# Optimization experiments

Measured on AMD Instinct MI355X. Metric: run time of the kernel, lower is better.

Reference implementation:

```python
import jax, jax.numpy as jnp
import numpy as np

LEAKY_SLOPE = 0.01
BN_EPS = 1e-5


def _local_conv(x, w, b, stride):
    # x: [B,C,H,W]; w: [1,O,C,OH,OW,K] (K = kh*kw, kh==kw); b: [1,O,OH,OW]
    sh, sw = stride
    _, O, C, oh, ow, K = w.shape
    k = int(round(K ** 0.5))
    # gather unfold patches: torch .unfold(2,kh,dh).unfold(3,kw,dw) -> last dim ordered (i major, j minor)
    patches = jnp.stack(
        [x[:, :, i:i + sh * oh:sh, j:j + sw * ow:sw] for i in range(k) for j in range(k)],
        axis=-1)  # [B,C,oh,ow,K]
    out = jnp.einsum('bchwk,ochwk->bohw', patches, w[0])
    return out + b  # b broadcasts [1,O,OH,OW]


def _bn_train(x, gamma, beta):
    # BatchNorm2d in training mode: biased batch statistics over (N,H,W)
    m = jnp.mean(x, axis=(0, 2, 3), keepdims=True)
    v = jnp.var(x, axis=(0, 2, 3), keepdims=True)
    return gamma[None, :, None, None] * (x - m) * jax.lax.rsqrt(v + BN_EPS) + beta[None, :, None, None]


def _lrelu(x):
    return jnp.where(x >= 0, x, LEAKY_SLOPE * x)


def _pad1(x):
    return jnp.pad(x, ((0, 0), (0, 0), (1, 1), (1, 1)))


def setup_inputs() -> dict:
    key = jax.random.key(0)
    ks = jax.random.split(key, 16)
    B = 8192
    inp = {
        'image': jax.random.normal(ks[0], (B, 10, 9, 1), jnp.float32),
        'conv1_w': jax.random.normal(ks[1], (64, 1, 2, 2), jnp.float32) * 0.5,
        'conv1_b': jax.random.normal(ks[2], (64,), jnp.float32) * 0.1,
        'lc1_w': jax.random.normal(ks[3], (1, 16, 64, 10, 5, 9), jnp.float32) * 0.05,
        'lc1_b': jax.random.normal(ks[4], (1, 16, 10, 5), jnp.float32) * 0.1,
        'lc2_w': jax.random.normal(ks[5], (1, 8, 16, 11, 6, 4), jnp.float32) * 0.1,
        'lc2_b': jax.random.normal(ks[6], (1, 8, 11, 6), jnp.float32) * 0.1,
        'lc3_w': jax.random.normal(ks[7], (1, 8, 8, 12, 4, 4), jnp.float32) * 0.1,
        'lc3_b': jax.random.normal(ks[8], (1, 8, 12, 4), jnp.float32) * 0.1,
        'gamma1': jax.random.normal(ks[9], (16,), jnp.float32) * 0.1 + 1.0,
        'beta1': jax.random.normal(ks[10], (16,), jnp.float32) * 0.1,
        'gamma2': jax.random.normal(ks[11], (8,), jnp.float32) * 0.1 + 1.0,
        'beta2': jax.random.normal(ks[12], (8,), jnp.float32) * 0.1,
        'gamma3': jax.random.normal(ks[13], (8,), jnp.float32) * 0.1 + 1.0,
        'beta3': jax.random.normal(ks[14], (8,), jnp.float32) * 0.1,
    }
    return inp


def reference(image, conv1_w, conv1_b, lc1_w, lc1_b, lc2_w, lc2_b, lc3_w, lc3_b,
              gamma1, beta1, gamma2, beta2, gamma3, beta3):
    x = jnp.transpose(image, (0, 3, 1, 2))  # [B,1,10,9]
    # Conv2d kernel 2, padding='same' (torch pads extra on right/bottom for even kernels)
    x = jax.lax.conv_general_dilated(
        x, conv1_w, window_strides=(1, 1), padding=[(0, 1), (0, 1)],
        dimension_numbers=('NCHW', 'OIHW', 'NCHW'))
    x = x + conv1_b[None, :, None, None]
    x = _lrelu(x)
    x = _pad1(x)                               # [B,64,12,11]
    x = _local_conv(x, lc1_w, lc1_b, (1, 2))   # [B,16,10,5]
    x = _lrelu(x)
    x = _bn_train(x, gamma1, beta1)
    x = _pad1(x)                               # [B,16,12,7]
    x = _local_conv(x, lc2_w, lc2_b, (1, 1))   # [B,8,11,6]
    x = _lrelu(x)
    x = _bn_train(x, gamma2, beta2)
    x = _pad1(x)                               # [B,8,13,8]
    x = _local_conv(x, lc3_w, lc3_b, (1, 2))   # [B,8,12,4]
    x = _lrelu(x)
    x = _bn_train(x, gamma3, beta3)
    return x.reshape(x.shape[0], -1)           # [B,384]
```

## Files before the change

### kernel.cpp

```cpp
#include <hip/hip_runtime.h>


typedef float  f32x4 __attribute__((ext_vector_type(4)));
typedef float  f32x2 __attribute__((ext_vector_type(2)));
typedef short  bf16x8 __attribute__((ext_vector_type(8)));

union FR  { int4 i4; bf16x8 bf; unsigned u[4]; };

#define LRELU(v) fmaxf((v), 0.01f * (v))

static __device__ inline unsigned bfr(float f) {
    unsigned u = __float_as_uint(f);
    return (u + 0x7fffu + ((u >> 16) & 1u)) >> 16;
}
static __device__ inline unsigned short bfr16(float f) { return (unsigned short)bfr(f); }
static __device__ inline float ubf(unsigned lo16) { return __uint_as_float(lo16 << 16); }

#if __has_builtin(__builtin_elementwise_fma)
static __device__ inline f32x2 pk_fma(f32x2 a, f32x2 b, f32x2 c) { return __builtin_elementwise_fma(a, b, c); }
#else
static __device__ inline f32x2 pk_fma(f32x2 a, f32x2 b, f32x2 c) { return a * b + c; }
#endif
static __device__ inline f32x2 pk_lrelu(f32x2 v) {
#if __has_builtin(__builtin_elementwise_max)
    return __builtin_elementwise_max(v, v * 0.01f);
#else
    f32x2 r; r.x = LRELU(v.x); r.y = LRELU(v.y); return r;
#endif
}
static __device__ inline float aload(float* p) {
    return __hip_atomic_load(p, __ATOMIC_RELAXED, __HIP_MEMORY_SCOPE_AGENT);
}

union PrepSM { float imgP[16][110]; float wt[9216]; };

__global__ __launch_bounds__(256) void kprep(
    const float* __restrict__ imgp,
    const float* __restrict__ cw,
    const float* __restrict__ cb,
    const float* __restrict__ lw1,
    unsigned* __restrict__ x1u,
    int4* __restrict__ afg1, float* __restrict__ stats,
    int nA, int doAux, int spp)
{
    __shared__ PrepSM sm;
    const int bx = blockIdx.x, tid = threadIdx.x;

    if (bx < nA) {
        const int sb = bx * 16;
        for (int e = tid; e < 1760; e += 256) ((float*)sm.imgP)[e] = 0.0f;
        __syncthreads();
        for (int e = tid; e < 1440; e += 256) {
            int s = e / 90, hw = e - s * 90;
            int r = hw / 9, c = hw - r * 9;
            sm.imgP[s][r * 10 + c] = imgp[(size_t)sb * 90 + e];
        }
        __syncthreads();

        const int quad = tid & 3, s = (tid >> 2) & 15;
        const int h = (tid >> 6) & 1, hwo = tid >> 7;
        const int ch0 = h * 32 + quad * 8;
        f32x2 W00[4], W01[4], W10[4], W11[4], BB[4];
        #pragma unroll
        for (int p = 0; p < 4; ++p) {
            int ca = ch0 + 2 * p, cbn = ca + 1;
            W00[p] = (f32x2){cw[ca * 4 + 0], cw[cbn * 4 + 0]};
            W01[p] = (f32x2){cw[ca * 4 + 1], cw[cbn * 4 + 1]};
            W10[p] = (f32x2){cw[ca * 4 + 2], cw[cbn * 4 + 2]};
            W11[p] = (f32x2){cw[ca * 4 + 3], cw[cbn * 4 + 3]};
            BB[p]  = (f32x2){cb[ca], cb[cbn]};
        }
        const float* ip = sm.imgP[s];
        uint4* x1q = (uint4*)x1u;
        #pragma unroll 3
        for (int it = 0; it < 45; ++it) {
            int hw = it * 2 + hwo;
            int r = hw / 9, c = hw - r * 9;
            float i00 = ip[r * 10 + c],      i01 = ip[r * 10 + c + 1];
            float i10 = ip[r * 10 + c + 10], i11 = ip[r * 10 + c + 11];
            unsigned u[4];
            #pragma unroll
            for (int p = 0; p < 4; ++p) {
                f32x2 v = BB[p];
                v = pk_fma((f32x2)i00, W00[p], v);
                v = pk_fma((f32x2)i01, W01[p], v);
                v = pk_fma((f32x2)i10, W10[p], v);
                v = pk_fma((f32x2)i11, W11[p], v);
                v = pk_lrelu(v);
                u[p] = bfr(v.x) | (bfr(v.y) << 16);
            }
            x1q[((size_t)(hw * 2 + h) * spp + (sb + s)) * 4 + quad] =
                make_uint4(u[0], u[1], u[2], u[3]);
        }
        return;
    }
    if (!doAux) return;

    const int b2 = bx - nA;
    if (b2 < 50) {
        const int pos = b2;
        for (int e = tid; e < 9216; e += 256) {
            int pair = e / 9, t = e - 9 * pair;
            sm.wt[e] = lw1[pair * 450 + pos * 9 + t];
        }
        __syncthreads();
        for (int e = tid; e < 1152; e += 256) {
            int l = e & 63, ht = e >> 6;
            int h = (ht >= 9) ? 1 : 0, t = ht - 9 * h;
            int q = l >> 4, o = l & 15;
            unsigned uu[4];
            #pragma unroll
            for (int p = 0; p < 4; ++p) {
                int c0 = 32 * h + 8 * q + 2 * p;
                float a0 = sm.wt[(o * 64 + c0) * 9 + t];
                float a1 = sm.wt[(o * 64 + c0 + 1) * 9 + t];
                uu[p] = bfr(a0) | (bfr(a1) << 16);
            }
            int4 st = { (int)uu[0], (int)uu[1], (int)uu[2], (int)uu[3] };
            afg1[pos * 1152 + e] = st;
        }
    } else if (tid < 64) stats[tid] = 0.0f;
}

__global__ __launch_bounds__(256) void k1_lc1(
    const int4* __restrict__ x1v,
    const int4* __restrict__ afg,
    const float* __restrict__ lb,
    unsigned short* __restrict__ y1b,
    float* __restrict__ stats,
    int sampOff, int spp, int nc)
{
    __shared__ int4  AfL[1216];
    __shared__ float bl[16];
    __shared__ float red[32];

    int pos, chunk;
    {
        int id = blockIdx.x;
        if (nc >= 8) { int k8 = id & 7; int r = id >> 3; pos = r % 50; chunk = (r / 50) * 8 + k8; }
        else         { pos = id % 50; chunk = id / 50; }
    }
    const int oh = pos / 5, ow = pos % 5;
    const int tid = threadIdx.x;
    const int wv = tid >> 6, lane = tid & 63;
    const int lane15 = lane & 15, q = lane >> 4;

    for (int e = tid; e < 1152; e += 256) AfL[e] = afg[pos * 1152 + e];
    if (tid < 64) AfL[1152 + tid] = (int4){0, 0, 0, 0};
    if (tid < 16) bl[tid] = lb[tid * 50 + pos];
    if (tid < 32) red[tid] = 0.0f;
    __syncthreads();

    const int sLoc = chunk * 256 + wv * 64;
    const int sAbs = sampOff + sLoc;
    const int spp4 = spp * 4;

    int sb0[9], af0[9], af1[9];
    #pragma unroll
    for (int t = 0; t < 9; ++t) {
        int ti = t / 3, tj = t % 3;
        int r = oh + ti - 1, c2 = 2 * ow + tj - 1;
        bool ok = (r >= 0 && r < 10 && c2 >= 0 && c2 < 9);
        int hw = ok ? (r * 9 + c2) : 0;
        sb0[t] = hw * 2 * spp4;
        af0[t] = ok ? t * 64 : 1152;
        af1[t] = ok ? (9 + t) * 64 : 1152;
    }

    f32x4 acc[4];
    #pragma unroll
    for (int g = 0; g < 4; ++g) {
        const int bg = (sLoc + g * 16 + lane15) * 4 + q;
        FR fb[9][2];
        #pragma unroll
        for (int t = 0; t < 9; ++t) {
            fb[t][0].i4 = x1v[sb0[t] + bg];
            fb[t][1].i4 = x1v[sb0[t] + spp4 + bg];
        }
        f32x4 a = (f32x4){0.f, 0.f, 0.f, 0.f};
        #pragma unroll
        for (int t = 0; t < 9; ++t) {
            FR fa0; fa0.i4 = AfL[af0[t] + lane];
            a = __builtin_amdgcn_mfma_f32_16x16x32_bf16(fa0.bf, fb[t][0].bf, a, 0, 0, 0);
            FR fa1; fa1.i4 = AfL[af1[t] + lane];
            a = __builtin_amdgcn_mfma_f32_16x16x32_bf16(fa1.bf, fb[t][1].bf, a, 0, 0, 0);
        }
        acc[g] = a;
    }

    float so[4] = {0, 0, 0, 0}, sq[4] = {0, 0, 0, 0};
    #pragma unroll
    for (int g = 0; g < 4; ++g)
        #pragma unroll
        for (int r = 0; r < 4; ++r) {
            int o = q * 4 + r;
            float v = acc[g][r] + bl[o];
            v = LRELU(v);
            y1b[(size_t)(o * 50 + pos) * 8192 + sAbs + g * 16 + lane15] = bfr16(v);
            so[r] += v; sq[r] += v * v;
        }
    #pragma unroll
    for (int r = 0; r < 4; ++r) {
        #pragma unroll
        for (int m = 1; m < 16; m <<= 1) {
            so[r] += __shfl_xor(so[r], m, 16);
            sq[r] += __shfl_xor(sq[r], m, 16);
        }
        if (lane15 == 0) {
            int o = q * 4 + r;
            atomicAdd(&red[o], so[r]);
            atomicAdd(&red[16 + o], sq[r]);
        }
    }
    __syncthreads();
    if (tid < 32) atomicAdd(&stats[tid], red[tid]);
}

__global__ __launch_bounds__(256) void k2_lc2(
    const unsigned short* __restrict__ y1b,
    const float* __restrict__ lw2, const float* __restrict__ lb2,
    const float* __restrict__ g1, const float* __restrict__ be1,
    unsigned short* __restrict__ y2b, float* __restrict__ stats)
{
    __shared__ float wld[512];
    __shared__ float a1[16], b1[16], bl[8], red[16];

    const int unit = blockIdx.x;
    const int pos = unit >> 3, chunk = unit & 7;
    const int oh = pos / 6, ow = pos % 6;
    const int tid = threadIdx.x, lane = tid & 63;

    if (tid < 128) {
        const float* src = lw2 + tid * 264 + pos * 4;
        int o = tid >> 4, c = tid & 15;
        #pragma unroll
        for (int k = 0; k < 4; k++) wld[c * 32 + k * 8 + o] = src[k];
    }
    if (tid < 16) {
        float m = aload(&stats[tid]) * (1.0f / 409600.0f);
        float v = aload(&stats[16 + tid]) * (1.0f / 409600.0f) - m * m;
        float a = g1[tid] * rsqrtf(v + 1e-5f);
        a1[tid] = a; b1[tid] = be1[tid] - a * m;
        if (tid < 8) bl[tid] = lb2[tid * 66 + pos];
        red[tid] = 0.0f;
    }
    __syncthreads();

    int base[4]; float kmv[4];
    #pragma unroll
    for (int i = 0; i < 2; i++)
        #pragma unroll
        for (int j = 0; j < 2; j++) {
            int r = oh + i - 1, c2 = ow + j - 1;
            bool ok = (r >= 0 && r < 10 && c2 >= 0 && c2 < 5);
            int rc = min(max(r, 0), 9), cc2 = min(max(c2, 0), 4);
            base[i * 2 + j] = rc * 5 + cc2;
            kmv[i * 2 + j] = ok ? 1.0f : 0.0f;
        }

    const int sb = chunk * 1024 + tid * 4;
    float acc[8][4];
    #pragma unroll
    for (int o = 0; o < 8; o++)
        #pragma unroll
        for (int s = 0; s < 4; s++) acc[o][s] = bl[o];

    #pragma unroll 1
    for (int c = 0; c < 16; c++) {
        float av = a1[c], bv = b1[c];
        float p[4][4];
        #pragma unroll
        for (int t = 0; t < 4; t++) {
            float ap = av * kmv[t], bp = bv * kmv[t];
            uint2 U = *(const uint2*)(y1b + (size_t)(c * 50 + base[t]) * 8192 + sb);
            p[t][0] = fmaf(ap, ubf(U.x & 0xffffu), bp);
            p[t][1] = fmaf(ap, __uint_as_float(U.x & 0xffff0000u), bp);
            p[t][2] = fmaf(ap, ubf(U.y & 0xffffu), bp);
            p[t][3] = fmaf(ap, __uint_as_float(U.y & 0xffff0000u), bp);
        }
        const float4* wr = (const float4*)&wld[c * 32];
        #pragma unroll
        for (int t = 0; t < 4; t++) {
            float4 wa = wr[t * 2], wb = wr[t * 2 + 1];
            #pragma unroll
            for (int s = 0; s < 4; s++) {
                float pv = p[t][s];
                acc[0][s] += wa.x * pv; acc[1][s] += wa.y * pv;
                acc[2][s] += wa.z * pv; acc[3][s] += wa.w * pv;
                acc[4][s] += wb.x * pv; acc[5][s] += wb.y * pv;
                acc[6][s] += wb.z * pv; acc[7][s] += wb.w * pv;
            }
        }
    }

    #pragma unroll
    for (int o = 0; o < 8; o++) {
        float v0 = LRELU(acc[o][0]), v1 = LRELU(acc[o][1]);
        float v2 = LRELU(acc[o][2]), v3 = LRELU(acc[o][3]);
        uint2 st = { bfr(v0) | (bfr(v1) << 16), bfr(v2) | (bfr(v3) << 16) };
        *(uint2*)(y2b + (size_t)(o * 66 + pos) * 8192 + sb) = st;
        float sv = v0 + v1 + v2 + v3;
        float sqv = v0 * v0 + v1 * v1 + v2 * v2 + v3 * v3;
        #pragma unroll
        for (int m = 32; m > 0; m >>= 1) {
            sv  += __shfl_xor(sv, m, 64);
            sqv += __shfl_xor(sqv, m, 64);
        }
        if (lane == 0) { atomicAdd(&red[o], sv); atomicAdd(&red[8 + o], sqv); }
    }
    __syncthreads();
    if (tid < 16) atomicAdd(&stats[32 + tid], red[tid]);
}

__global__ __launch_bounds__(256) void k3_lc3(
    const unsigned short* __restrict__ y2b,
    const float* __restrict__ lw3, const float* __restrict__ lb3,
    const float* __restrict__ g2, const float* __restrict__ be2,
    unsigned short* __restrict__ y3b, float* __restrict__ stats)
{
    __shared__ float wld[256];
    __shared__ float a2[8], b2[8], bl[8], red[16];

    const int unit = blockIdx.x;
    const int pos = unit >> 3, chunk = unit & 7;
    const int oh = pos >> 2, ow = pos & 3;
    const int tid = threadIdx.x, lane = tid & 63;

    if (tid < 64) {
        const float* src = lw3 + tid * 192 + pos * 4;
        int o = tid >> 3, c = tid & 7;
        #pragma unroll
        for (int k = 0; k < 4; k++) wld[c * 32 + k * 8 + o] = src[k];
    }
    if (tid < 16) {
        if (tid < 8) {
            float m = aload(&stats[32 + tid]) * (1.0f / 540672.0f);
            float v = aload(&stats[40 + tid]) * (1.0f / 540672.0f) - m * m;
            float a = g2[tid] * rsqrtf(v + 1e-5f);
            a2[tid] = a; b2[tid] = be2[tid] - a * m;
            bl[tid] = lb3[tid * 48 + pos];
        }
        red[tid] = 0.0f;
    }
    __syncthreads();

    int base[4]; float kmv[4];
    #pragma unroll
    for (int i = 0; i < 2; i++)
        #pragma unroll
        for (int j = 0; j < 2; j++) {
            int r = oh + i - 1, c2 = 2 * ow + j - 1;
            bool ok = (r >= 0 && r < 11 && c2 >= 0 && c2 < 6);
            int rc = min(max(r, 0), 10), cc2 = min(max(c2, 0), 5);
            base[i * 2 + j] = rc * 6 + cc2;
            kmv[i * 2 + j] = ok ? 1.0f : 0.0f;
        }

    const int sb = chunk * 1024 + tid * 4;
    float acc[8][4];
    #pragma unroll
    for (int o = 0; o < 8; o++)
        #pragma unroll
        for (int s = 0; s < 4; s++) acc[o][s] = bl[o];

    #pragma unroll 1
    for (int c = 0; c < 8; c++) {
        float av = a2[c], bv = b2[c];
        float p[4][4];
        #pragma unroll
        for (int t = 0; t < 4; t++) {
            float ap = av * kmv[t], bp = bv * kmv[t];
            uint2 U = *(const uint2*)(y2b + (size_t)(c * 66 + base[t]) * 8192 + sb);
            p[t][0] = fmaf(ap, ubf(U.x & 0xffffu), bp);
            p[t][1] = fmaf(ap, __uint_as_float(U.x & 0xffff0000u), bp);
            p[t][2] = fmaf(ap, ubf(U.y & 0xffffu), bp);
            p[t][3] = fmaf(ap, __uint_as_float(U.y & 0xffff0000u), bp);
        }
        const float4* wr = (const float4*)&wld[c * 32];
        #pragma unroll
        for (int t = 0; t < 4; t++) {
            float4 wa = wr[t * 2], wb = wr[t * 2 + 1];
            #pragma unroll
            for (int s = 0; s < 4; s++) {
                float pv = p[t][s];
                acc[0][s] += wa.x * pv; acc[1][s] += wa.y * pv;
                acc[2][s] += wa.z * pv; acc[3][s] += wa.w * pv;
                acc[4][s] += wb.x * pv; acc[5][s] += wb.y * pv;
                acc[6][s] += wb.z * pv; acc[7][s] += wb.w * pv;
            }
        }
    }

    #pragma unroll
    for (int o = 0; o < 8; o++) {
        float v0 = LRELU(acc[o][0]), v1 = LRELU(acc[o][1]);
        float v2 = LRELU(acc[o][2]), v3 = LRELU(acc[o][3]);
        uint2 st = { bfr(v0) | (bfr(v1) << 16), bfr(v2) | (bfr(v3) << 16) };
        *(uint2*)(y3b + (size_t)(o * 48 + pos) * 8192 + sb) = st;
        float sv = v0 + v1 + v2 + v3;
        float sqv = v0 * v0 + v1 * v1 + v2 * v2 + v3 * v3;
        #pragma unroll
        for (int m = 32; m > 0; m >>= 1) {
            sv  += __shfl_xor(sv, m, 64);
            sqv += __shfl_xor(sqv, m, 64);
        }
        if (lane == 0) { atomicAdd(&red[o], sv); atomicAdd(&red[8 + o], sqv); }
    }
    __syncthreads();
    if (tid < 16) atomicAdd(&stats[48 + tid], red[tid]);
}

__global__ __launch_bounds__(256) void k4_out(
    const unsigned short* __restrict__ y3b,
    const float* __restrict__ g3, const float* __restrict__ be3,
    float* __restrict__ stats, float* __restrict__ out)
{
    __shared__ unsigned short tile[64][66];
    __shared__ float a3[8], b3[8];
    const int unit = blockIdx.x;
    const int tid = threadIdx.x;
    const int chunkS = unit & 31, yy = unit >> 5;
    const int ftile = yy >> 2, sub = yy & 3;
    const int fbase = ftile * 64;
    const int sbase = chunkS * 256 + sub * 64;

    if (tid < 8) {
        float m = aload(&stats[48 + tid]) * (1.0f / 393216.0f);
        float v = aload(&stats[56 + tid]) * (1.0f / 393216.0f) - m * m;
        float a = g3[tid] * rsqrtf(v + 1e-5f);
        a3[tid] = a; b3[tid] = be3[tid] - a * m;
    }
    __syncthreads();

    #pragma unroll
    for (int rep = 0; rep < 16; rep++) {
        int idx = rep * 256 + tid;
        int f = idx >> 6, s = idx & 63;
        tile[f][s] = y3b[(size_t)(fbase + f) * 8192 + sbase + s];
    }
    __syncthreads();
    #pragma unroll
    for (int rep = 0; rep < 16; rep++) {
        int idx = rep * 256 + tid;
        int s = idx >> 6, f = idx & 63;
        int ff = fbase + f;
        int o = ff / 48;
        float x = ubf((unsigned)tile[f][s]);
        out[(size_t)(sbase + s) * 384 + ff] = a3[o] * x + b3[o];
    }
}

extern "C" void kernel_launch(void* const* d_in, const int* in_sizes, int n_in,
                              void* d_out, int out_size, void* d_ws, size_t ws_size,
                              hipStream_t stream) {
    const float* image   = (const float*)d_in[0];
    const float* conv1_w = (const float*)d_in[1];
    const float* conv1_b = (const float*)d_in[2];
    const float* lc1_w   = (const float*)d_in[3];
    const float* lc1_b   = (const float*)d_in[4];
    const float* lc2_w   = (const float*)d_in[5];
    const float* lc2_b   = (const float*)d_in[6];
    const float* lc3_w   = (const float*)d_in[7];
    const float* lc3_b   = (const float*)d_in[8];
    const float* gamma1  = (const float*)d_in[9];
    const float* beta1   = (const float*)d_in[10];
    const float* gamma2  = (const float*)d_in[11];
    const float* beta2   = (const float*)d_in[12];
    const float* gamma3  = (const float*)d_in[13];
    const float* beta3   = (const float*)d_in[14];
    float* outp = (float*)d_out;

    char* wsb = (char*)d_ws;
    float*          stats = (float*)wsb;
    unsigned short* y1b   = (unsigned short*)(wsb + 1024);
    int4*           afg1  = (int4*)(wsb + 13108224);
    char*           x1reg = wsb + 14029824;
    unsigned short* y2b   = (unsigned short*)(wsb + 14029824);
    unsigned short* y3b   = (unsigned short*)(wsb + 22680576);

    const size_t bytesPerSamp = 11520;
    int nPass = 1;
    if (ws_size < 14029824ul + 8192ul * bytesPerSamp) nPass = 2;
    if (ws_size < 14029824ul + 4096ul * bytesPerSamp) nPass = 4;
    if (ws_size < 14029824ul + 2048ul * bytesPerSamp) nPass = 8;
    const int spp = 8192 / nPass;
    const int nA  = spp / 16;
    const int nc  = spp / 256;

    unsigned*   x1u = (unsigned*)x1reg;
    const int4* x1v = (const int4*)x1reg;

    for (int p = 0; p < nPass; ++p) {
        const float* imgp = image + (size_t)p * spp * 90;
        kprep<<<dim3(p == 0 ? nA + 51 : nA), dim3(256), 0, stream>>>(
            imgp, conv1_w, conv1_b, lc1_w, x1u, afg1, stats, nA, p == 0 ? 1 : 0, spp);
        k1_lc1<<<dim3(50 * nc), dim3(256), 0, stream>>>(
            x1v, afg1, lc1_b, y1b, stats, p * spp, spp, nc);
    }
    k2_lc2<<<dim3(528), dim3(256), 0, stream>>>(y1b, lc2_w, lc2_b,
                                                gamma1, beta1, y2b, stats);
    k3_lc3<<<dim3(384), dim3(256), 0, stream>>>(y2b, lc3_w, lc3_b,
                                                gamma2, beta2, y3b, stats);
    k4_out<<<dim3(768), dim3(256), 0, stream>>>(y3b, gamma3, beta3, stats, outp);
}
```

Baseline: 193.7 us.

## Stream lc1 activation slices through a per-wave LDS ring via async global-to-LDS loads

```diff
diff --git a/kernel.cpp b/kernel.cpp
--- a/kernel.cpp
+++ b/kernel.cpp
@@ -8,6 +8,7 @@
 union FR  { int4 i4; bf16x8 bf; unsigned u[4]; };
 
 #define LRELU(v) fmaxf((v), 0.01f * (v))
+#define WAITVM(n) asm volatile("s_waitcnt vmcnt(" #n ")" ::: "memory")
 
 static __device__ inline unsigned bfr(float f) {
     unsigned u = __float_as_uint(f);
@@ -30,6 +31,11 @@
 }
 static __device__ inline float aload(float* p) {
     return __hip_atomic_load(p, __ATOMIC_RELAXED, __HIP_MEMORY_SCOPE_AGENT);
+}
+static __device__ __forceinline__ void dma16(const void* g, void* l) {
+    __builtin_amdgcn_global_load_lds(
+        (const __attribute__((address_space(1))) void*)g,
+        (__attribute__((address_space(3))) void*)l, 16, 0, 0);
 }
 
 union PrepSM { float imgP[16][110]; float wt[9216]; };
@@ -123,14 +129,14 @@
 }
 
 __global__ __launch_bounds__(256) void k1_lc1(
-    const int4* __restrict__ x1v,
+    const unsigned char* __restrict__ x1base,
     const int4* __restrict__ afg,
     const float* __restrict__ lb,
     unsigned short* __restrict__ y1b,
     float* __restrict__ stats,
     int sampOff, int spp, int nc)
 {
-    __shared__ int4  AfL[1216];
+    __shared__ __align__(16) unsigned char ring[4][4][4096];
     __shared__ float bl[16];
     __shared__ float red[32];
 
@@ -145,47 +151,79 @@
     const int wv = tid >> 6, lane = tid & 63;
     const int lane15 = lane & 15, q = lane >> 4;
 
-    for (int e = tid; e < 1152; e += 256) AfL[e] = afg[pos * 1152 + e];
-    if (tid < 64) AfL[1152 + tid] = (int4){0, 0, 0, 0};
     if (tid < 16) bl[tid] = lb[tid * 50 + pos];
     if (tid < 32) red[tid] = 0.0f;
     __syncthreads();
 
-    const int sLoc = chunk * 256 + wv * 64;
-    const int sAbs = sampOff + sLoc;
-    const int spp4 = spp * 4;
-
-    int sb0[9], af0[9], af1[9];
+    FR fa[18];
+    int slabOf[18];
+    const int sliceStride = spp * 64;
     #pragma unroll
     for (int t = 0; t < 9; ++t) {
         int ti = t / 3, tj = t % 3;
         int r = oh + ti - 1, c2 = 2 * ow + tj - 1;
         bool ok = (r >= 0 && r < 10 && c2 >= 0 && c2 < 9);
         int hw = ok ? (r * 9 + c2) : 0;
-        sb0[t] = hw * 2 * spp4;
-        af0[t] = ok ? t * 64 : 1152;
-        af1[t] = ok ? (9 + t) * 64 : 1152;
+        #pragma unroll
+        for (int h = 0; h < 2; ++h) {
+            int s = 2 * t + h;
+            slabOf[s] = (hw * 2 + h) * sliceStride;
+            if (ok) fa[s].i4 = afg[pos * 1152 + (h * 9 + t) * 64 + lane];
+            else    fa[s].i4 = (int4){0, 0, 0, 0};
+        }
+    }
+
+    const int sLoc = chunk * 256 + wv * 64;
+    const int sAbs = sampOff + sLoc;
+    const unsigned char* slicePtr = x1base + (size_t)sLoc * 64;
+
+    int gOffL[4];
+    #pragma unroll
+    for (int i = 0; i < 4; ++i) {
+        int u = i * 64 + lane;
+        int sampL = u >> 2;
+        int qqG = (u & 3) ^ ((sampL >> 1) & 3);
+        gOffL[i] = sampL * 64 + qqG * 16;
+    }
+    int offB[4];
+    #pragma unroll
+    for (int g = 0; g < 4; ++g) {
+        int s2 = g * 16 + lane15;
+        offB[g] = (s2 * 4 + (q ^ ((s2 >> 1) & 3))) * 16;
+    }
+
+    WAITVM(0);
+
+    #pragma unroll
+    for (int s = 0; s < 4; ++s) {
+        const unsigned char* sp = slicePtr + slabOf[s];
+        #pragma unroll
+        for (int i = 0; i < 4; ++i)
+            dma16(sp + gOffL[i], &ring[wv][s][i * 1024]);
     }
 
     f32x4 acc[4];
     #pragma unroll
-    for (int g = 0; g < 4; ++g) {
-        const int bg = (sLoc + g * 16 + lane15) * 4 + q;
-        FR fb[9][2];
-        #pragma unroll
-        for (int t = 0; t < 9; ++t) {
-            fb[t][0].i4 = x1v[sb0[t] + bg];
-            fb[t][1].i4 = x1v[sb0[t] + spp4 + bg];
-        }
-        f32x4 a = (f32x4){0.f, 0.f, 0.f, 0.f};
-        #pragma unroll
-        for (int t = 0; t < 9; ++t) {
-            FR fa0; fa0.i4 = AfL[af0[t] + lane];
-            a = __builtin_amdgcn_mfma_f32_16x16x32_bf16(fa0.bf, fb[t][0].bf, a, 0, 0, 0);
-            FR fa1; fa1.i4 = AfL[af1[t] + lane];
-            a = __builtin_amdgcn_mfma_f32_16x16x32_bf16(fa1.bf, fb[t][1].bf, a, 0, 0, 0);
-        }
-        acc[g] = a;
+    for (int g = 0; g < 4; ++g) acc[g] = (f32x4){0.f, 0.f, 0.f, 0.f};
+
+    #pragma unroll
+    for (int s = 0; s < 18; ++s) {
+        if (s < 15)      { WAITVM(12); }
+        else if (s == 15){ WAITVM(8);  }
+        else if (s == 16){ WAITVM(4);  }
+        else             { WAITVM(0);  }
+        const int slot = s & 3;
+        #pragma unroll
+        for (int g = 0; g < 4; ++g) {
+            FR fb; fb.i4 = *(const int4*)&ring[wv][slot][offB[g]];
+            acc[g] = __builtin_amdgcn_mfma_f32_16x16x32_bf16(fa[s].bf, fb.bf, acc[g], 0, 0, 0);
+        }
+        if (s + 4 < 18) {
+            const unsigned char* sp = slicePtr + slabOf[s + 4];
+            #pragma unroll
+            for (int i = 0; i < 4; ++i)
+                dma16(sp + gOffL[i], &ring[wv][slot][i * 1024]);
+        }
     }
 
     float so[4] = {0, 0, 0, 0}, sq[4] = {0, 0, 0, 0};
@@ -487,15 +525,14 @@
     const int nA  = spp / 16;
     const int nc  = spp / 256;
 
-    unsigned*   x1u = (unsigned*)x1reg;
-    const int4* x1v = (const int4*)x1reg;
+    unsigned* x1u = (unsigned*)x1reg;
 
     for (int p = 0; p < nPass; ++p) {
         const float* imgp = image + (size_t)p * spp * 90;
         kprep<<<dim3(p == 0 ? nA + 51 : nA), dim3(256), 0, stream>>>(
             imgp, conv1_w, conv1_b, lc1_w, x1u, afg1, stats, nA, p == 0 ? 1 : 0, spp);
         k1_lc1<<<dim3(50 * nc), dim3(256), 0, stream>>>(
-            x1v, afg1, lc1_b, y1b, stats, p * spp, spp, nc);
+            (const unsigned char*)x1reg, afg1, lc1_b, y1b, stats, p * spp, spp, nc);
     }
     k2_lc2<<<dim3(528), dim3(256), 0, stream>>>(y1b, lc2_w, lc2_b,
                                                 gamma1, beta1, y2b, stats);
```

After: 192.9 us. About the same (-0.4%).
